# Performance work log

Hardware: AMD Instinct MI355X
Metric: run time of the kernel (lower is better)

Reference implementation:

```python
import jax, jax.numpy as jnp
import numpy as np

N_NODES = 100000
N_EDGES = 1600000
F_IN = 512
D_EMB = 128
D_HID = 64
N_CLS = 32
EPS = 1e-5


def setup_inputs() -> dict:
    key = jax.random.key(0)
    ks = jax.random.split(key, 16)
    def w(k, shape):
        fan_in = shape[0]
        return jax.random.normal(k, shape, dtype=jnp.float32) / jnp.sqrt(jnp.float32(fan_in))
    return {
        "x": jax.random.normal(ks[0], (N_NODES, F_IN), dtype=jnp.float32),
        "W1": w(ks[1], (F_IN, D_EMB)), "b1": jnp.zeros((D_EMB,), jnp.float32),
        "Wc1": w(ks[2], (D_EMB, D_HID)), "bc1": jnp.zeros((D_HID,), jnp.float32),
        "Wc2": w(ks[3], (D_HID, D_HID)), "bc2": jnp.zeros((D_HID,), jnp.float32),
        "Wc3": w(ks[4], (D_HID, D_HID)), "bc3": jnp.zeros((D_HID,), jnp.float32),
        "gamma": jnp.ones((D_HID,), jnp.float32), "beta": jnp.zeros((D_HID,), jnp.float32),
        "W2": w(ks[5], (D_HID, N_CLS)), "b2": jnp.zeros((N_CLS,), jnp.float32),
        "W3": w(ks[6], (N_CLS, N_CLS)), "b3": jnp.zeros((N_CLS,), jnp.float32),
        "edge_index": jax.random.randint(ks[7], (2, N_EDGES), 0, N_NODES, dtype=jnp.int32),
    }


def _agg_mean(h, src, dst, n):
    # gather source-node features along edges, sum into destination nodes, divide by degree
    s = jax.ops.segment_sum(h[src], dst, num_segments=n)          # [N, d]
    deg = jax.ops.segment_sum(jnp.ones((src.shape[0], 1), h.dtype), dst, num_segments=n)
    return s / jnp.maximum(deg, 1.0)


def _conv1p(h, src, dst, W, b):
    # ConvolutionalLayer_1P: neighborhood gather/aggregate -> linear -> relu
    return jax.nn.relu(_agg_mean(h, src, dst, h.shape[0]) @ W + b)


def reference(x, W1, b1, Wc1, bc1, Wc2, bc2, Wc3, bc3, gamma, beta, W2, b2, W3, b3, edge_index):
    src, dst = edge_index[0], edge_index[1]
    # linmaps1 on 0th-order ptensors == identity copy
    h = jax.nn.relu(x @ W1 + b1)                 # lin1 + relu (dropout = identity in eval)
    h = _conv1p(h, src, dst, Wc1, bc1)           # conv1
    h = _conv1p(h, src, dst, Wc2, bc2)           # conv2
    h = _conv1p(h, src, dst, Wc3, bc3)           # conv3
    mean = jnp.mean(h, axis=0)
    var = jnp.var(h, axis=0)
    h = (h - mean) * jax.lax.rsqrt(var + EPS) * gamma + beta  # batchnorm (batch stats)
    h = jax.nn.relu(h @ W2 + b2)                 # lin2 + relu (dropout = identity)
    out = h @ W3 + b3                            # lin3; linmaps0 == identity
    return out
```

## Files before the change

### kernel.cpp

```cpp
#include <hip/hip_runtime.h>
#include <cstdint>
#include <cstddef>

constexpr int F_IN  = 512;
constexpr int D_EMB = 128;
constexpr int D_HID = 64;
constexpr int N_CLS = 32;

typedef __attribute__((ext_vector_type(8))) short short8;
typedef __attribute__((ext_vector_type(4))) float floatx4;

__device__ inline unsigned short f2bf(float f) {
  union { float f; uint32_t u; } v; v.f = f;
  uint32_t r = v.u + 0x7FFF + ((v.u >> 16) & 1);
  return (unsigned short)(r >> 16);
}

__device__ inline uint32_t pack2bf(float lo, float hi) {
  return ((uint32_t)f2bf(hi) << 16) | (uint32_t)f2bf(lo);
}

__global__ __launch_bounds__(256) void wt_kernel(
    const float* __restrict__ W1, short8* __restrict__ Wt2)
{
  int idx = blockIdx.x * 256 + threadIdx.x;
  int kc8 = idx >> 10, lin = idx & 1023;
  int ct = lin >> 7, rem = lin & 127, ks = rem >> 6, ln = rem & 63;
  int col = ct * 16 + (ln & 15);
  int k0 = kc8 * 64 + ks * 32 + (ln >> 4) * 8;
  short8 s;
#pragma unroll
  for (int j = 0; j < 8; ++j)
    s[j] = (short)f2bf(W1[(size_t)(k0 + j) * D_EMB + col]);
  Wt2[idx] = s;
}

__global__ __launch_bounds__(256) void l1c1_kernel(
    const float* __restrict__ X, const short8* __restrict__ Wt2,
    const float* __restrict__ b1, const float* __restrict__ Wc1,
    unsigned short* __restrict__ P, int n)
{
  __shared__ __align__(16) char smem[50176];
  short8* Xs = (short8*)smem;
  short8* Ws = (short8*)(smem + 8192);
  float (*Hs)[132] = (float(*)[132])smem;
  float (*Wc)[64]  = (float(*)[64])(smem + 33792);

  const int t = threadIdx.x;
  const int wave = t >> 6, lane = t & 63;
  const int quad = lane >> 4, mrow = lane & 15;
  const int node0 = blockIdx.x * 64;
  const int cw = wave * 2;

  float4 wp[4];
#pragma unroll
  for (int i = 0; i < 4; ++i) wp[i] = ((const float4*)Wc1)[i * 256 + t];

  const float* sp[2];
  int soff[2];
#pragma unroll
  for (int i = 0; i < 2; ++i) {
    int g = t + i * 256;
    int row = g >> 3, col8 = g & 7;
    soff[i] = row * 128 + ((col8 * 16) ^ ((row & 7) << 4));
    int gr = node0 + row; if (gr >= n) gr = n - 1;
    sp[i] = &X[(size_t)gr * F_IN + col8 * 8];
  }

  floatx4 acc[4][2];
#pragma unroll
  for (int i = 0; i < 4; ++i)
#pragma unroll
    for (int j = 0; j < 2; ++j) acc[i][j] = (floatx4){0.f, 0.f, 0.f, 0.f};

  float4 xrA[2][2], xrB[2][2];
  short8 wrA[4], wrB[4];

#pragma unroll
  for (int i = 0; i < 2; ++i) {
    xrA[i][0] = *(const float4*)sp[i];
    xrA[i][1] = *(const float4*)(sp[i] + 4);
    xrB[i][0] = *(const float4*)(sp[i] + 64);
    xrB[i][1] = *(const float4*)(sp[i] + 68);
  }
#pragma unroll
  for (int i = 0; i < 4; ++i) {
    wrA[i] = Wt2[t + i * 256];
    wrB[i] = Wt2[1024 + t + i * 256];
  }

  auto substep = [&](float4 (&xr)[2][2], short8 (&wr)[4], int knext) {
    short8 s8[2];
#pragma unroll
    for (int i = 0; i < 2; ++i) {
      s8[i][0] = (short)f2bf(xr[i][0].x); s8[i][1] = (short)f2bf(xr[i][0].y);
      s8[i][2] = (short)f2bf(xr[i][0].z); s8[i][3] = (short)f2bf(xr[i][0].w);
      s8[i][4] = (short)f2bf(xr[i][1].x); s8[i][5] = (short)f2bf(xr[i][1].y);
      s8[i][6] = (short)f2bf(xr[i][1].z); s8[i][7] = (short)f2bf(xr[i][1].w);
    }
    __syncthreads();
#pragma unroll
    for (int i = 0; i < 2; ++i)
      *(short8*)((char*)Xs + soff[i]) = s8[i];
#pragma unroll
    for (int i = 0; i < 4; ++i)
      Ws[t + i * 256] = wr[i];
    __syncthreads();

    if (knext < 8) {
#pragma unroll
      for (int i = 0; i < 2; ++i) {
        const float* p = sp[i] + knext * 64;
        xr[i][0] = *(const float4*)p;
        xr[i][1] = *(const float4*)(p + 4);
      }
#pragma unroll
      for (int i = 0; i < 4; ++i)
        wr[i] = Wt2[knext * 1024 + t + i * 256];
    }

#pragma unroll
    for (int ks = 0; ks < 2; ++ks) {
      short8 af[4], bf[2];
#pragma unroll
      for (int rt = 0; rt < 4; ++rt) {
        int row = rt * 16 + mrow;
        int byteoff = row * 128 + ((ks * 64 + quad * 16) ^ ((row & 7) << 4));
        af[rt] = *(const short8*)((const char*)Xs + byteoff);
      }
#pragma unroll
      for (int c = 0; c < 2; ++c)
        bf[c] = Ws[((cw + c) * 2 + ks) * 64 + lane];
#pragma unroll
      for (int rt = 0; rt < 4; ++rt)
#pragma unroll
        for (int c = 0; c < 2; ++c)
          acc[rt][c] = __builtin_amdgcn_mfma_f32_16x16x32_bf16(
              af[rt], bf[c], acc[rt][c], 0, 0, 0);
    }
  };

#pragma unroll 1
  for (int kc8 = 0; kc8 < 8; kc8 += 2) {
    substep(xrA, wrA, kc8 + 2);
    substep(xrB, wrB, kc8 + 3);
  }

  __syncthreads();
#pragma unroll
  for (int ct = 0; ct < 2; ++ct) {
    int col = (cw + ct) * 16 + mrow;
    float b = b1[col];
#pragma unroll
    for (int rt = 0; rt < 4; ++rt)
#pragma unroll
      for (int r = 0; r < 4; ++r)
        Hs[rt * 16 + quad * 4 + r][col] = fmaxf(acc[rt][ct][r] + b, 0.f);
  }
#pragma unroll
  for (int i = 0; i < 4; ++i)
    ((float4*)&Wc[0][0])[i * 256 + t] = wp[i];
  __syncthreads();

#pragma unroll
  for (int i = 0; i < 4; ++i)
    wp[i] = ((const float4*)Wc1)[1024 + i * 256 + t];

  const int rg = t >> 4, cg = t & 15;
  float acc2[4][4];
#pragma unroll
  for (int i = 0; i < 4; ++i)
#pragma unroll
    for (int j = 0; j < 4; ++j) acc2[i][j] = 0.f;

#pragma unroll 8
  for (int k = 0; k < 64; ++k) {
    float a[4] = {Hs[rg*4+0][k], Hs[rg*4+1][k], Hs[rg*4+2][k], Hs[rg*4+3][k]};
    float4 b = *(const float4*)&Wc[k][cg * 4];
#pragma unroll
    for (int i = 0; i < 4; ++i) {
      acc2[i][0] += a[i]*b.x; acc2[i][1] += a[i]*b.y;
      acc2[i][2] += a[i]*b.z; acc2[i][3] += a[i]*b.w;
    }
  }
  __syncthreads();
#pragma unroll
  for (int i = 0; i < 4; ++i)
    ((float4*)&Wc[0][0])[i * 256 + t] = wp[i];
  __syncthreads();

#pragma unroll 8
  for (int k = 0; k < 64; ++k) {
    float a[4] = {Hs[rg*4+0][64+k], Hs[rg*4+1][64+k],
                  Hs[rg*4+2][64+k], Hs[rg*4+3][64+k]};
    float4 b = *(const float4*)&Wc[k][cg * 4];
#pragma unroll
    for (int i = 0; i < 4; ++i) {
      acc2[i][0] += a[i]*b.x; acc2[i][1] += a[i]*b.y;
      acc2[i][2] += a[i]*b.z; acc2[i][3] += a[i]*b.w;
    }
  }
#pragma unroll
  for (int i = 0; i < 4; ++i) {
    int gn = node0 + rg * 4 + i;
    if (gn < n) {
      uint2 o;
      o.x = pack2bf(acc2[i][0], acc2[i][1]);
      o.y = pack2bf(acc2[i][2], acc2[i][3]);
      *(uint2*)&P[(size_t)gn * 64 + cg * 4] = o;
    }
  }
}

__device__ inline void gather4_bf(
    const unsigned short* __restrict__ P, const int* __restrict__ adj,
    int beg, int end, int g, int li, float c[4])
{
  c[0] = 0.f; c[1] = 0.f; c[2] = 0.f; c[3] = 0.f;
  if (end > beg) {
    int e1 = end - 1;
    for (int jj = beg + g; jj < end; jj += 32) {
#pragma unroll
      for (int k = 0; k < 8; ++k) {
        int e = jj + 4 * k;
        int ec = min(e, e1);
        int idx = adj[ec];
        uint2 u = *(const uint2*)&P[(size_t)idx * 64 + li * 4];
        bool p = e < end;
        c[0] += p ? __uint_as_float(u.x << 16) : 0.f;
        c[1] += p ? __uint_as_float(u.x & 0xFFFF0000u) : 0.f;
        c[2] += p ? __uint_as_float(u.y << 16) : 0.f;
        c[3] += p ? __uint_as_float(u.y & 0xFFFF0000u) : 0.f;
      }
    }
  }
#pragma unroll
  for (int i = 0; i < 4; ++i) {
    c[i] += __shfl_xor(c[i], 16, 64);
    c[i] += __shfl_xor(c[i], 32, 64);
  }
}

__device__ inline void gather4_f32(
    const float* __restrict__ P, const int* __restrict__ adj,
    int beg, int end, int g, int li, float c[4])
{
  c[0] = 0.f; c[1] = 0.f; c[2] = 0.f; c[3] = 0.f;
  if (end > beg) {
    int e1 = end - 1;
    for (int jj = beg + g; jj < end; jj += 32) {
#pragma unroll
      for (int k = 0; k < 8; ++k) {
        int e = jj + 4 * k;
        int ec = min(e, e1);
        int idx = adj[ec];
        float4 u = *(const float4*)&P[(size_t)idx * 64 + li * 4];
        bool p = e < end;
        c[0] += p ? u.x : 0.f;
        c[1] += p ? u.y : 0.f;
        c[2] += p ? u.z : 0.f;
        c[3] += p ? u.w : 0.f;
      }
    }
  }
#pragma unroll
  for (int i = 0; i < 4; ++i) {
    c[i] += __shfl_xor(c[i], 16, 64);
    c[i] += __shfl_xor(c[i], 32, 64);
  }
}

template<bool INBF, bool OUTBF>
__global__ __launch_bounds__(512) void gmm_kernel(
    const void* __restrict__ Pv, const int* __restrict__ offs,
    const int* __restrict__ adj, const int* __restrict__ deg,
    const float* __restrict__ bin, const float* __restrict__ W,
    void* __restrict__ Outv, int n)
{
  __shared__ float Hs[64][68];
  __shared__ float Ws[64][64];
  __shared__ int offss[65];
  const int t = threadIdx.x;
  const int wave = t >> 6, lane = t & 63;
  const int g = lane >> 4, li = lane & 15;
  const int node0 = blockIdx.x * 64;

#pragma unroll
  for (int i = 0; i < 2; ++i) {
    int lin = t + i * 512;
    ((float4*)&Ws[0][0])[lin] = ((const float4*)W)[lin];
  }
  if (t < 65) offss[t] = offs[min(node0 + t, n)];
  __syncthreads();

  const float4 bb = *(const float4*)&bin[li * 4];

#pragma unroll 1
  for (int nd = 0; nd < 8; ++nd) {
    int ln = wave * 8 + nd;
    int node = node0 + ln;
    if (node < n) {
      float c[4];
      if (INBF)
        gather4_bf((const unsigned short*)Pv, adj, offss[ln], offss[ln + 1],
                   g, li, c);
      else
        gather4_f32((const float*)Pv, adj, offss[ln], offss[ln + 1],
                    g, li, c);
      float rd = 1.f / fmaxf((float)deg[node], 1.f);
      float4 v = make_float4(fmaxf(c[0] * rd + bb.x, 0.f),
                             fmaxf(c[1] * rd + bb.y, 0.f),
                             fmaxf(c[2] * rd + bb.z, 0.f),
                             fmaxf(c[3] * rd + bb.w, 0.f));
      if (g == 0) *(float4*)&Hs[ln][li * 4] = v;
    } else if (g == 0) {
      *(float4*)&Hs[ln][li * 4] = make_float4(0.f, 0.f, 0.f, 0.f);
    }
  }
  __syncthreads();

  const int rg = t >> 4, cg = t & 15;
  float acc[2][4];
#pragma unroll
  for (int i = 0; i < 2; ++i)
#pragma unroll
    for (int j = 0; j < 4; ++j) acc[i][j] = 0.f;

#pragma unroll 8
  for (int k = 0; k < 64; ++k) {
    float a[2] = {Hs[rg * 2 + 0][k], Hs[rg * 2 + 1][k]};
    float4 b = *(const float4*)&Ws[k][cg * 4];
#pragma unroll
    for (int i = 0; i < 2; ++i) {
      acc[i][0] += a[i]*b.x; acc[i][1] += a[i]*b.y;
      acc[i][2] += a[i]*b.z; acc[i][3] += a[i]*b.w;
    }
  }
#pragma unroll
  for (int i = 0; i < 2; ++i) {
    int gn = node0 + rg * 2 + i;
    if (gn < n) {
      if (OUTBF) {
        uint2 o;
        o.x = pack2bf(acc[i][0], acc[i][1]);
        o.y = pack2bf(acc[i][2], acc[i][3]);
        *(uint2*)&((unsigned short*)Outv)[(size_t)gn * 64 + cg * 4] = o;
      } else {
        float4 o = make_float4(acc[i][0], acc[i][1], acc[i][2], acc[i][3]);
        *(float4*)&((float*)Outv)[(size_t)gn * 64 + cg * 4] = o;
      }
    }
  }
}

__global__ __launch_bounds__(512) void gp_kernel(
    const float* __restrict__ P, const int* __restrict__ offs,
    const int* __restrict__ adj, const int* __restrict__ deg,
    const float* __restrict__ bc3, float* __restrict__ H4,
    float* __restrict__ stats, int n)
{
  __shared__ int offss[65];
  const int t = threadIdx.x;
  const int wave = t >> 6, lane = t & 63;
  const int g = lane >> 4, li = lane & 15;
  const int node0 = blockIdx.x * 64;
  if (t < 65) offss[t] = offs[min(node0 + t, n)];
  __syncthreads();

  const float4 bb = *(const float4*)&bc3[li * 4];
  float s[4] = {0.f, 0.f, 0.f, 0.f}, q[4] = {0.f, 0.f, 0.f, 0.f};

#pragma unroll 1
  for (int nd = 0; nd < 8; ++nd) {
    int ln = wave * 8 + nd;
    int node = node0 + ln;
    if (node >= n) break;
    float c[4];
    gather4_f32(P, adj, offss[ln], offss[ln + 1], g, li, c);
    float rd = 1.f / fmaxf((float)deg[node], 1.f);
    float4 v = make_float4(fmaxf(c[0] * rd + bb.x, 0.f),
                           fmaxf(c[1] * rd + bb.y, 0.f),
                           fmaxf(c[2] * rd + bb.z, 0.f),
                           fmaxf(c[3] * rd + bb.w, 0.f));
    if (g == 0) *(float4*)&H4[(size_t)node * 64 + li * 4] = v;
    s[0] += v.x; s[1] += v.y; s[2] += v.z; s[3] += v.w;
    q[0] += v.x*v.x; q[1] += v.y*v.y; q[2] += v.z*v.z; q[3] += v.w*v.w;
  }

  __shared__ float red[2][8][64];
  if (g == 0) {
    *(float4*)&red[0][wave][li * 4] = make_float4(s[0], s[1], s[2], s[3]);
    *(float4*)&red[1][wave][li * 4] = make_float4(q[0], q[1], q[2], q[3]);
  }
  __syncthreads();
  if (t < 128) {
    int which = t >> 6, ff = t & 63;
    float a = 0.f;
#pragma unroll
    for (int w = 0; w < 8; ++w) a += red[which][w][ff];
    atomicAdd(&stats[which * 64 + ff], a);
  }
}

__global__ __launch_bounds__(256) void hist_kernel(
    const int* __restrict__ dst, int* __restrict__ G,
    float* __restrict__ stats, int nE, int B, int NB)
{
  __shared__ int h[256];
  int blk = blockIdx.x, t = threadIdx.x;
  if (blk == 0 && t < 128) stats[t] = 0.f;
  h[t] = 0;
  __syncthreads();
  int base = blk * 8192;
  int lim = min(8192, nE - base);
  for (int i = t; i < lim; i += 256)
    atomicAdd(&h[dst[base + i] >> 9], 1);
  __syncthreads();
  if (t < NB) G[t * B + blk] = h[t];
}

__global__ __launch_bounds__(256) void scan1_kernel(
    const int* __restrict__ in, int* __restrict__ out,
    int* __restrict__ bsum, int n)
{
  __shared__ int sh[256];
  int t = threadIdx.x;
  int i = blockIdx.x * 256 + t;
  int c = (i < n) ? in[i] : 0;
  sh[t] = c;
  __syncthreads();
#pragma unroll
  for (int off = 1; off < 256; off <<= 1) {
    int v = 0;
    if (t >= off) v = sh[t - off];
    __syncthreads();
    if (t >= off) sh[t] += v;
    __syncthreads();
  }
  if (i < n) out[i] = sh[t] - c;
  if (t == 255) bsum[blockIdx.x] = sh[255];
}

__global__ __launch_bounds__(256) void scan2_kernel(int* __restrict__ bsum, int nb)
{
  __shared__ int sh[256];
  __shared__ int carry;
  int t = threadIdx.x;
  if (t == 0) carry = 0;
  __syncthreads();
  for (int base = 0; base < nb; base += 256) {
    int i = base + t;
    int v = (i < nb) ? bsum[i] : 0;
    sh[t] = v;
    __syncthreads();
#pragma unroll
    for (int off = 1; off < 256; off <<= 1) {
      int u = 0;
      if (t >= off) u = sh[t - off];
      __syncthreads();
      if (t >= off) sh[t] += u;
      __syncthreads();
    }
    int c0 = carry;
    int incl = sh[t], total = sh[255];
    if (i < nb) bsum[i] = c0 + incl - v;
    __syncthreads();
    if (t == 0) carry = c0 + total;
    __syncthreads();
  }
  if (t == 0) bsum[nb] = carry;
}

__global__ __launch_bounds__(256) void scatter2_kernel(
    const int* __restrict__ src, const int* __restrict__ dst,
    const int* __restrict__ W, const int* __restrict__ bsum,
    int2* __restrict__ EP, int nE, int B, int NB)
{
  __shared__ int cur[256];
  int blk = blockIdx.x, t = threadIdx.x;
  if (t < NB) {
    int gi = t * B + blk;
    cur[t] = W[gi] + bsum[gi >> 8];
  }
  __syncthreads();
  int base = blk * 8192;
  int lim = min(8192, nE - base);
  for (int i = t; i < lim; i += 256) {
    int s = src[base + i], d = dst[base + i];
    int slot = atomicAdd(&cur[d >> 9], 1);
    EP[slot] = make_int2(s, d);
  }
}

__global__ __launch_bounds__(256) void fillc_kernel(
    const int2* __restrict__ EP, const int* __restrict__ W,
    const int* __restrict__ bsum,
    int* __restrict__ cnt, int* __restrict__ offs, int* __restrict__ adj,
    int n, int nE, int B, int NB)
{
  __shared__ int h[512];
  int b = blockIdx.x, t = threadIdx.x;
  int g0i = b * B;
  int segStart = W[g0i] + bsum[g0i >> 8];
  int segEnd = (b == NB - 1) ? nE : (W[g0i + B] + bsum[(g0i + B) >> 8]);
  int nodeBase = b << 9;

  h[t] = 0; h[t + 256] = 0;
  __syncthreads();
  for (int i = segStart + t; i < segEnd; i += 256)
    atomicAdd(&h[EP[i].y - nodeBase], 1);
  __syncthreads();
  int c0 = h[t], c1 = h[t + 256];
#pragma unroll
  for (int off = 1; off < 512; off <<= 1) {
    int a = (t >= off) ? h[t - off] : 0;
    int bb = (t + 256 >= off) ? h[t + 256 - off] : 0;
    __syncthreads();
    h[t] += a; h[t + 256] += bb;
    __syncthreads();
  }
  int e0 = h[t] - c0, e1 = h[t + 256] - c1;
  int g0 = nodeBase + t, g1 = nodeBase + t + 256;
  if (g0 < n) { cnt[g0] = c0; offs[g0] = segStart + e0; }
  if (g1 < n) { cnt[g1] = c1; offs[g1] = segStart + e1; }
  if (b == 0 && t == 0) offs[n] = nE;
  __syncthreads();
  h[t] = e0; h[t + 256] = e1;
  __syncthreads();
  for (int i = segStart + t; i < segEnd; i += 256) {
    int2 p = EP[i];
    int slot = atomicAdd(&h[p.y - nodeBase], 1);
    adj[segStart + slot] = p.x;
  }
}

__global__ __launch_bounds__(256) void fold_kernel(
    const float* __restrict__ stats, const float* __restrict__ gamma,
    const float* __restrict__ beta, const float* __restrict__ W2,
    const float* __restrict__ b2, float* __restrict__ W2f,
    float* __restrict__ b2f, int n)
{
  __shared__ float rsg[64], corr[64];
  int t = threadIdx.x;
  if (t < 64) {
    float m = stats[t] / (float)n;
    float var = stats[64 + t] / (float)n - m * m;
    float rs = rsqrtf(var + 1e-5f);
    float g = gamma[t] * rs;
    rsg[t] = g;
    corr[t] = beta[t] - m * g;
  }
  __syncthreads();
#pragma unroll
  for (int i = 0; i < 8; ++i) {
    int lin = t + i * 256;
    int k = lin >> 5;
    W2f[lin] = rsg[k] * W2[lin];
  }
  if (t < 32) {
    float a = b2[t];
    for (int k = 0; k < 64; ++k) a += corr[k] * W2[k * 32 + t];
    b2f[t] = a;
  }
}

__global__ __launch_bounds__(256) void final_kernel(
    const float* __restrict__ H4, const float* __restrict__ W2f,
    const float* __restrict__ b2f, const float* __restrict__ W3,
    const float* __restrict__ b3, float* __restrict__ Out, int n)
{
  __shared__ float Hs[64][68];
  __shared__ float W2s[64][32];
  __shared__ float W3s[32][32];
  __shared__ float Us[64][36];
  __shared__ float b2s[32], b3s[32];
  const int t = threadIdx.x;
  const int node0 = blockIdx.x * 64;

#pragma unroll
  for (int i = 0; i < 4; ++i) {
    int lin = t + i * 256;
    int node = lin >> 4, kq = lin & 15;
    float4 v = make_float4(0.f, 0.f, 0.f, 0.f);
    if (node0 + node < n)
      v = *(const float4*)&H4[(size_t)(node0 + node) * 64 + kq * 4];
    *(float4*)&Hs[node][kq * 4] = v;
  }
#pragma unroll
  for (int i = 0; i < 2; ++i) {
    int lin = t + i * 256;
    ((float4*)&W2s[0][0])[lin] = ((const float4*)W2f)[lin];
  }
  ((float4*)&W3s[0][0])[t & 255] = ((const float4*)W3)[t & 255];
  if (t < 32) { b2s[t] = b2f[t]; b3s[t] = b3[t]; }
  __syncthreads();

  const int rg = t >> 4, cg = t & 15;
  float acc[4][2] = {{0.f,0.f},{0.f,0.f},{0.f,0.f},{0.f,0.f}};
#pragma unroll 8
  for (int k = 0; k < 64; ++k) {
    float a[4] = {Hs[rg*4+0][k], Hs[rg*4+1][k], Hs[rg*4+2][k], Hs[rg*4+3][k]};
    float w0 = W2s[k][cg*2], w1 = W2s[k][cg*2+1];
#pragma unroll
    for (int i = 0; i < 4; ++i) { acc[i][0] += a[i]*w0; acc[i][1] += a[i]*w1; }
  }
#pragma unroll
  for (int i = 0; i < 4; ++i) {
    Us[rg*4+i][cg*2+0] = fmaxf(acc[i][0] + b2s[cg*2+0], 0.f);
    Us[rg*4+i][cg*2+1] = fmaxf(acc[i][1] + b2s[cg*2+1], 0.f);
  }
  __syncthreads();

  float acc2[4][2] = {{0.f,0.f},{0.f,0.f},{0.f,0.f},{0.f,0.f}};
#pragma unroll
  for (int k = 0; k < 32; ++k) {
    float a[4] = {Us[rg*4+0][k], Us[rg*4+1][k], Us[rg*4+2][k], Us[rg*4+3][k]};
    float w0 = W3s[k][cg*2], w1 = W3s[k][cg*2+1];
#pragma unroll
    for (int i = 0; i < 4; ++i) { acc2[i][0] += a[i]*w0; acc2[i][1] += a[i]*w1; }
  }
  float (*Os)[36] = (float(*)[36])Hs;
#pragma unroll
  for (int i = 0; i < 4; ++i) {
    Os[rg*4+i][cg*2+0] = acc2[i][0] + b3s[cg*2+0];
    Os[rg*4+i][cg*2+1] = acc2[i][1] + b3s[cg*2+1];
  }
  __syncthreads();
#pragma unroll
  for (int i = 0; i < 2; ++i) {
    int lin = t + i * 256;
    int node = lin >> 3, c4 = lin & 7;
    if (node0 + node < n)
      *(float4*)&Out[(size_t)(node0 + node) * 32 + c4 * 4] =
          *(float4*)&Os[node][c4 * 4];
  }
}

extern "C" void kernel_launch(void* const* d_in, const int* in_sizes, int n_in,
                              void* d_out, int out_size, void* d_ws, size_t ws_size,
                              hipStream_t stream)
{
  const float* X     = (const float*)d_in[0];
  const float* W1    = (const float*)d_in[1];
  const float* b1    = (const float*)d_in[2];
  const float* Wc1   = (const float*)d_in[3];
  const float* bc1   = (const float*)d_in[4];
  const float* Wc2   = (const float*)d_in[5];
  const float* bc2   = (const float*)d_in[6];
  const float* Wc3   = (const float*)d_in[7];
  const float* bc3   = (const float*)d_in[8];
  const float* gamma = (const float*)d_in[9];
  const float* beta  = (const float*)d_in[10];
  const float* W2    = (const float*)d_in[11];
  const float* b2    = (const float*)d_in[12];
  const float* W3    = (const float*)d_in[13];
  const float* b3    = (const float*)d_in[14];
  const int*   ei    = (const int*)d_in[15];

  const int n  = in_sizes[0] / F_IN;
  const int nE = in_sizes[15] / 2;
  const int* src  = ei;
  const int* dstv = ei + nE;

  const int NB = (n + 511) >> 9;
  const int B  = (nE + 8191) >> 13;
  const int NG = NB * B;
  const int nbG = (NG + 255) / 256;

  char* wsb = (char*)d_ws;
  unsigned short* Pa = (unsigned short*)wsb;
  unsigned short* Pb = (unsigned short*)(wsb + (size_t)n * 128);
  float* Pc    = (float*)(wsb + (size_t)n * 256);
  float* H4    = (float*)(wsb + (size_t)n * 512);
  float* stats = H4 + (size_t)n * 64;
  float* W2f   = stats + 128;
  float* b2f   = W2f + 2048;
  int*   cnt   = (int*)(b2f + 32);
  int*   offs  = cnt + n;
  int*   G     = offs + n + 1;
  int*   W     = G + NG;
  int*   bsum  = W + NG + 1;
  int*   adj   = bsum + nbG + 1;
  uintptr_t epAddr = ((uintptr_t)(adj + nE) + 7) & ~(uintptr_t)7;
  int2*  EP    = (int2*)epAddr;
  short8* Wt2  = (short8*)(EP + nE);

  const int nb  = (n + 63) / 64;

  wt_kernel<<<32, 256, 0, stream>>>(W1, Wt2);
  l1c1_kernel<<<nb, 256, 0, stream>>>(X, Wt2, b1, Wc1, Pa, n);

  hist_kernel<<<B, 256, 0, stream>>>(dstv, G, stats, nE, B, NB);
  scan1_kernel<<<nbG, 256, 0, stream>>>(G, W, bsum, NG);
  scan2_kernel<<<1, 256, 0, stream>>>(bsum, nbG);
  scatter2_kernel<<<B, 256, 0, stream>>>(src, dstv, W, bsum, EP, nE, B, NB);
  fillc_kernel<<<NB, 256, 0, stream>>>(EP, W, bsum, cnt, offs, adj, n, nE, B, NB);

  gmm_kernel<true, true><<<nb, 512, 0, stream>>>(
      Pa, offs, adj, cnt, bc1, Wc2, Pb, n);

  gmm_kernel<true, false><<<nb, 512, 0, stream>>>(
      Pb, offs, adj, cnt, bc2, Wc3, Pc, n);

  gp_kernel<<<nb, 512, 0, stream>>>(Pc, offs, adj, cnt, bc3, H4, stats, n);

  fold_kernel<<<1, 256, 0, stream>>>(stats, gamma, beta, W2, b2, W2f, b2f, n);
  final_kernel<<<nb, 256, 0, stream>>>(H4, W2f, b2f, W3, b3, (float*)d_out, n);
}
```

Baseline: 665.1 us.

## Narrow bf16 gather lanes, pack edge pairs into one int, derive degree from offsets

The bf16 neighbor gather now maps 32 lanes across the 64 features with 4-byte loads and two edge groups per wave instead of four, and the f32 gather's unroll is cut to 4. Edge (src,dst) pairs are packed into a single int (src<<9 | local dst), which halves the scratch traffic of the CSR build. Degree is computed from the CSR offsets, so the separate cnt array and its loads are dropped. The packing assumes node ids fit in 23 bits, and fewer edges are in flight per wave, which may reduce latency hiding in the gather.

```diff
diff --git a/kernel.cpp b/kernel.cpp
--- a/kernel.cpp
+++ b/kernel.cpp
@@ -212,45 +212,42 @@
   }
 }
 
-__device__ inline void gather4_bf(
+__device__ inline void gather2_bf(
     const unsigned short* __restrict__ P, const int* __restrict__ adj,
-    int beg, int end, int g, int li, float c[4])
+    int beg, int end, int g, int li, float& c0, float& c1)
+{
+  c0 = 0.f; c1 = 0.f;
+  if (end > beg) {
+    int e1 = end - 1;
+    for (int jj = beg + g; jj < end; jj += 16) {
+#pragma unroll
+      for (int k = 0; k < 8; ++k) {
+        int e = jj + 2 * k;
+        int ec = min(e, e1);
+        int idx = adj[ec];
+        uint32_t u = *(const uint32_t*)&P[(size_t)idx * 64 + li * 2];
+        float lo = __uint_as_float(u << 16);
+        float hi = __uint_as_float(u & 0xFFFF0000u);
+        bool p = e < end;
+        c0 += p ? lo : 0.f;
+        c1 += p ? hi : 0.f;
+      }
+    }
+  }
+  c0 += __shfl_xor(c0, 32, 64);
+  c1 += __shfl_xor(c1, 32, 64);
+}
+
+__device__ inline void gather4_f32(
+    const float* __restrict__ P, const int* __restrict__ adj,
+    int beg, int end, int g4, int li, float c[4])
 {
   c[0] = 0.f; c[1] = 0.f; c[2] = 0.f; c[3] = 0.f;
   if (end > beg) {
     int e1 = end - 1;
-    for (int jj = beg + g; jj < end; jj += 32) {
-#pragma unroll
-      for (int k = 0; k < 8; ++k) {
-        int e = jj + 4 * k;
-        int ec = min(e, e1);
-        int idx = adj[ec];
-        uint2 u = *(const uint2*)&P[(size_t)idx * 64 + li * 4];
-        bool p = e < end;
-        c[0] += p ? __uint_as_float(u.x << 16) : 0.f;
-        c[1] += p ? __uint_as_float(u.x & 0xFFFF0000u) : 0.f;
-        c[2] += p ? __uint_as_float(u.y << 16) : 0.f;
-        c[3] += p ? __uint_as_float(u.y & 0xFFFF0000u) : 0.f;
-      }
-    }
-  }
-#pragma unroll
-  for (int i = 0; i < 4; ++i) {
-    c[i] += __shfl_xor(c[i], 16, 64);
-    c[i] += __shfl_xor(c[i], 32, 64);
-  }
-}
-
-__device__ inline void gather4_f32(
-    const float* __restrict__ P, const int* __restrict__ adj,
-    int beg, int end, int g, int li, float c[4])
-{
-  c[0] = 0.f; c[1] = 0.f; c[2] = 0.f; c[3] = 0.f;
-  if (end > beg) {
-    int e1 = end - 1;
-    for (int jj = beg + g; jj < end; jj += 32) {
-#pragma unroll
-      for (int k = 0; k < 8; ++k) {
+    for (int jj = beg + g4; jj < end; jj += 16) {
+#pragma unroll
+      for (int k = 0; k < 4; ++k) {
         int e = jj + 4 * k;
         int ec = min(e, e1);
         int idx = adj[ec];
@@ -270,10 +267,10 @@
   }
 }
 
-template<bool INBF, bool OUTBF>
+template<bool OUTBF>
 __global__ __launch_bounds__(512) void gmm_kernel(
-    const void* __restrict__ Pv, const int* __restrict__ offs,
-    const int* __restrict__ adj, const int* __restrict__ deg,
+    const unsigned short* __restrict__ P, const int* __restrict__ offs,
+    const int* __restrict__ adj,
     const float* __restrict__ bin, const float* __restrict__ W,
     void* __restrict__ Outv, int n)
 {
@@ -282,7 +279,7 @@
   __shared__ int offss[65];
   const int t = threadIdx.x;
   const int wave = t >> 6, lane = t & 63;
-  const int g = lane >> 4, li = lane & 15;
+  const int g = lane >> 5, li = lane & 31;
   const int node0 = blockIdx.x * 64;
 
 #pragma unroll
@@ -293,28 +290,22 @@
   if (t < 65) offss[t] = offs[min(node0 + t, n)];
   __syncthreads();
 
-  const float4 bb = *(const float4*)&bin[li * 4];
+  const float2 bb = *(const float2*)&bin[li * 2];
 
 #pragma unroll 1
   for (int nd = 0; nd < 8; ++nd) {
     int ln = wave * 8 + nd;
     int node = node0 + ln;
     if (node < n) {
-      float c[4];
-      if (INBF)
-        gather4_bf((const unsigned short*)Pv, adj, offss[ln], offss[ln + 1],
-                   g, li, c);
-      else
-        gather4_f32((const float*)Pv, adj, offss[ln], offss[ln + 1],
-                    g, li, c);
-      float rd = 1.f / fmaxf((float)deg[node], 1.f);
-      float4 v = make_float4(fmaxf(c[0] * rd + bb.x, 0.f),
-                             fmaxf(c[1] * rd + bb.y, 0.f),
-                             fmaxf(c[2] * rd + bb.z, 0.f),
-                             fmaxf(c[3] * rd + bb.w, 0.f));
-      if (g == 0) *(float4*)&Hs[ln][li * 4] = v;
+      float c0, c1;
+      int beg = offss[ln], end = offss[ln + 1];
+      gather2_bf(P, adj, beg, end, g, li, c0, c1);
+      float rd = 1.f / fmaxf((float)(end - beg), 1.f);
+      float v0 = fmaxf(c0 * rd + bb.x, 0.f);
+      float v1 = fmaxf(c1 * rd + bb.y, 0.f);
+      if (g == 0) *(float2*)&Hs[ln][li * 2] = make_float2(v0, v1);
     } else if (g == 0) {
-      *(float4*)&Hs[ln][li * 4] = make_float4(0.f, 0.f, 0.f, 0.f);
+      *(float2*)&Hs[ln][li * 2] = make_float2(0.f, 0.f);
     }
   }
   __syncthreads();
@@ -355,14 +346,14 @@
 
 __global__ __launch_bounds__(512) void gp_kernel(
     const float* __restrict__ P, const int* __restrict__ offs,
-    const int* __restrict__ adj, const int* __restrict__ deg,
+    const int* __restrict__ adj,
     const float* __restrict__ bc3, float* __restrict__ H4,
     float* __restrict__ stats, int n)
 {
   __shared__ int offss[65];
   const int t = threadIdx.x;
   const int wave = t >> 6, lane = t & 63;
-  const int g = lane >> 4, li = lane & 15;
+  const int g4 = lane >> 4, li = lane & 15;
   const int node0 = blockIdx.x * 64;
   if (t < 65) offss[t] = offs[min(node0 + t, n)];
   __syncthreads();
@@ -376,19 +367,20 @@
     int node = node0 + ln;
     if (node >= n) break;
     float c[4];
-    gather4_f32(P, adj, offss[ln], offss[ln + 1], g, li, c);
-    float rd = 1.f / fmaxf((float)deg[node], 1.f);
+    int beg = offss[ln], end = offss[ln + 1];
+    gather4_f32(P, adj, beg, end, g4, li, c);
+    float rd = 1.f / fmaxf((float)(end - beg), 1.f);
     float4 v = make_float4(fmaxf(c[0] * rd + bb.x, 0.f),
                            fmaxf(c[1] * rd + bb.y, 0.f),
                            fmaxf(c[2] * rd + bb.z, 0.f),
                            fmaxf(c[3] * rd + bb.w, 0.f));
-    if (g == 0) *(float4*)&H4[(size_t)node * 64 + li * 4] = v;
+    if (g4 == 0) *(float4*)&H4[(size_t)node * 64 + li * 4] = v;
     s[0] += v.x; s[1] += v.y; s[2] += v.z; s[3] += v.w;
     q[0] += v.x*v.x; q[1] += v.y*v.y; q[2] += v.z*v.z; q[3] += v.w*v.w;
   }
 
   __shared__ float red[2][8][64];
-  if (g == 0) {
+  if (g4 == 0) {
     *(float4*)&red[0][wave][li * 4] = make_float4(s[0], s[1], s[2], s[3]);
     *(float4*)&red[1][wave][li * 4] = make_float4(q[0], q[1], q[2], q[3]);
   }
@@ -474,7 +466,7 @@
 __global__ __launch_bounds__(256) void scatter2_kernel(
     const int* __restrict__ src, const int* __restrict__ dst,
     const int* __restrict__ W, const int* __restrict__ bsum,
-    int2* __restrict__ EP, int nE, int B, int NB)
+    int* __restrict__ EP, int nE, int B, int NB)
 {
   __shared__ int cur[256];
   int blk = blockIdx.x, t = threadIdx.x;
@@ -488,14 +480,14 @@
   for (int i = t; i < lim; i += 256) {
     int s = src[base + i], d = dst[base + i];
     int slot = atomicAdd(&cur[d >> 9], 1);
-    EP[slot] = make_int2(s, d);
+    EP[slot] = (s << 9) | (d & 511);
   }
 }
 
 __global__ __launch_bounds__(256) void fillc_kernel(
-    const int2* __restrict__ EP, const int* __restrict__ W,
+    const int* __restrict__ EP, const int* __restrict__ W,
     const int* __restrict__ bsum,
-    int* __restrict__ cnt, int* __restrict__ offs, int* __restrict__ adj,
+    int* __restrict__ offs, int* __restrict__ adj,
     int n, int nE, int B, int NB)
 {
   __shared__ int h[512];
@@ -508,7 +500,7 @@
   h[t] = 0; h[t + 256] = 0;
   __syncthreads();
   for (int i = segStart + t; i < segEnd; i += 256)
-    atomicAdd(&h[EP[i].y - nodeBase], 1);
+    atomicAdd(&h[EP[i] & 511], 1);
   __syncthreads();
   int c0 = h[t], c1 = h[t + 256];
 #pragma unroll
@@ -521,16 +513,16 @@
   }
   int e0 = h[t] - c0, e1 = h[t + 256] - c1;
   int g0 = nodeBase + t, g1 = nodeBase + t + 256;
-  if (g0 < n) { cnt[g0] = c0; offs[g0] = segStart + e0; }
-  if (g1 < n) { cnt[g1] = c1; offs[g1] = segStart + e1; }
+  if (g0 < n) offs[g0] = segStart + e0;
+  if (g1 < n) offs[g1] = segStart + e1;
   if (b == 0 && t == 0) offs[n] = nE;
   __syncthreads();
   h[t] = e0; h[t + 256] = e1;
   __syncthreads();
   for (int i = segStart + t; i < segEnd; i += 256) {
-    int2 p = EP[i];
-    int slot = atomicAdd(&h[p.y - nodeBase], 1);
-    adj[segStart + slot] = p.x;
+    int u = EP[i];
+    int slot = atomicAdd(&h[u & 511], 1);
+    adj[segStart + slot] = u >> 9;
   }
 }
 
@@ -675,15 +667,13 @@
   float* stats = H4 + (size_t)n * 64;
   float* W2f   = stats + 128;
   float* b2f   = W2f + 2048;
-  int*   cnt   = (int*)(b2f + 32);
-  int*   offs  = cnt + n;
+  int*   offs  = (int*)(b2f + 32);
   int*   G     = offs + n + 1;
   int*   W     = G + NG;
   int*   bsum  = W + NG + 1;
   int*   adj   = bsum + nbG + 1;
-  uintptr_t epAddr = ((uintptr_t)(adj + nE) + 7) & ~(uintptr_t)7;
-  int2*  EP    = (int2*)epAddr;
-  short8* Wt2  = (short8*)(EP + nE);
+  int*   EP    = adj + nE;
+  short8* Wt2  = (short8*)(((uintptr_t)(EP + nE) + 15) & ~(uintptr_t)15);
 
   const int nb  = (n + 63) / 64;
 
@@ -694,15 +684,13 @@
   scan1_kernel<<<nbG, 256, 0, stream>>>(G, W, bsum, NG);
   scan2_kernel<<<1, 256, 0, stream>>>(bsum, nbG);
   scatter2_kernel<<<B, 256, 0, stream>>>(src, dstv, W, bsum, EP, nE, B, NB);
-  fillc_kernel<<<NB, 256, 0, stream>>>(EP, W, bsum, cnt, offs, adj, n, nE, B, NB);
-
-  gmm_kernel<true, true><<<nb, 512, 0, stream>>>(
-      Pa, offs, adj, cnt, bc1, Wc2, Pb, n);
-
-  gmm_kernel<true, false><<<nb, 512, 0, stream>>>(
-      Pb, offs, adj, cnt, bc2, Wc3, Pc, n);
-
-  gp_kernel<<<nb, 512, 0, stream>>>(Pc, offs, adj, cnt, bc3, H4, stats, n);
+  fillc_kernel<<<NB, 256, 0, stream>>>(EP, W, bsum, offs, adj, n, nE, B, NB);
+
+  gmm_kernel<true><<<nb, 512, 0, stream>>>(Pa, offs, adj, bc1, Wc2, Pb, n);
+
+  gmm_kernel<false><<<nb, 512, 0, stream>>>(Pb, offs, adj, bc2, Wc3, Pc, n);
+
+  gp_kernel<<<nb, 512, 0, stream>>>(Pc, offs, adj, bc3, H4, stats, n);
 
   fold_kernel<<<1, 256, 0, stream>>>(stats, gamma, beta, W2, b2, W2f, b2f, n);
   final_kernel<<<nb, 256, 0, stream>>>(H4, W2f, b2f, W3, b3, (float*)d_out, n);
```

New measurement: 592.8 us. -10.9%, faster.
